# Kernel tuning notes

Measured on AMD Instinct MI355X. Metric: run time of the kernel, lower is better.

Reference implementation:

```python
import jax, jax.numpy as jnp
import numpy as np

B, S, D_IN, D_OUT = 8, 2048, 1024, 1024


def setup_inputs() -> dict:
    key = jax.random.key(0)
    kx, kq, kk, kv = jax.random.split(key, 4)
    x = jax.random.normal(kx, (B, S, D_IN), dtype=jnp.float32)
    # torch nn.Linear weight is (d_out, d_in); we store the transpose (d_in, d_out)
    # and apply as x @ W, same math. Scale ~ kaiming-uniform-ish magnitude.
    scale = 1.0 / np.sqrt(D_IN)
    Wq = jax.random.normal(kq, (D_IN, D_OUT), dtype=jnp.float32) * scale
    Wk = jax.random.normal(kk, (D_IN, D_OUT), dtype=jnp.float32) * scale
    Wv = jax.random.normal(kv, (D_IN, D_OUT), dtype=jnp.float32) * scale
    return {"x": x, "Wq": Wq, "Wk": Wk, "Wv": Wv}


def reference(x, Wq, Wk, Wv):
    # x: (b, s, d_in) -> (b, s, d_out). Single-head causal attention, dropout=0.
    b, s, _ = x.shape
    q = jnp.einsum('bsd,de->bse', x, Wq)
    k = jnp.einsum('bsd,de->bse', x, Wk)
    v = jnp.einsum('bsd,de->bse', x, Wv)
    d_k = k.shape[-1]
    scores = jnp.einsum('bqe,bke->bqk', q, k) / jnp.sqrt(jnp.float32(d_k))
    # causal mask: position t attends to 0..t (strict upper triangle -> -inf)
    causal = jnp.tril(jnp.ones((s, s), dtype=bool))
    scores = jnp.where(causal[None, :, :], scores, -jnp.inf)
    weights = jax.nn.softmax(scores, axis=-1)
    return jnp.einsum('bqk,bke->bqe', weights, v)
```

## Files before the change

### kernel.cpp

```cpp
#include <hip/hip_runtime.h>


#define Bv 8
#define Sv 2048
#define Dv 1024
#define BK 32

typedef _Float16 f16x8 __attribute__((ext_vector_type(8)));
typedef _Float16 f16x4 __attribute__((ext_vector_type(4)));
typedef float    f32x4 __attribute__((ext_vector_type(4)));

#define GLL(gp, lp)                                            \
  __builtin_amdgcn_global_load_lds(                            \
      (const __attribute__((address_space(1))) void*)(gp),     \
      (__attribute__((address_space(3))) void*)(lp), 16, 0, 0)

__device__ __forceinline__ void mma_step(const _Float16* As, const _Float16* Bs,
                                         int wm, int wn, int lane, f32x4 acc[4][4]) {
  int ll = lane & 15, quad = lane >> 4;
  f16x8 a[4], b[4];
#pragma unroll
  for (int mi = 0; mi < 4; ++mi)
    a[mi] = *(const f16x8*)(As + (wm * 64 + mi * 16 + ll) * BK + quad * 8);
#pragma unroll
  for (int ni = 0; ni < 4; ++ni)
    b[ni] = *(const f16x8*)(Bs + (wn * 64 + ni * 16 + ll) * BK + quad * 8);
#pragma unroll
  for (int mi = 0; mi < 4; ++mi)
#pragma unroll
    for (int ni = 0; ni < 4; ++ni)
      acc[mi][ni] = __builtin_amdgcn_mfma_f32_16x16x32_f16(a[mi], b[ni], acc[mi][ni], 0, 0, 0);
}

__device__ __forceinline__ void gemm_dbuf(const _Float16* __restrict__ A, int lda,
                                          const _Float16* __restrict__ B, int ldb,
                                          int ktiles, _Float16 (*S)[4096],
                                          f32x4 acc[4][4]) {
  const int tid  = threadIdx.x;
  const int lane = tid & 63, wave = tid >> 6;
  const int wm = wave >> 1, wn = wave & 1;
  const int srow = wave * 32 + (lane >> 2);
  const int scol = (lane & 3) * 8;
  const int loA0 = srow * lda + scol, loA1 = loA0 + 16 * lda;
  const int loB0 = srow * ldb + scol, loB1 = loB0 + 16 * ldb;
  _Float16* dA = &S[0][wave * 1024];
  _Float16* dB = &S[1][wave * 1024];
  const _Float16* gA = A;
  const _Float16* gB = B;

#define STAGE(bi)                              \
  do {                                         \
    GLL(gA + loA0, dA + (bi) * 8192);          \
    GLL(gA + loA1, dA + (bi) * 8192 + 512);    \
    GLL(gB + loB0, dB + (bi) * 8192);          \
    GLL(gB + loB1, dB + (bi) * 8192 + 512);    \
  } while (0)

  STAGE(0);
  for (int kt = 0; kt < ktiles; kt += 2) {
    __syncthreads();
    gA += BK; gB += BK;
    STAGE(1);
    mma_step(S[0], S[1], wm, wn, lane, acc);
    __syncthreads();
    gA += BK; gB += BK;
    if (kt + 2 < ktiles) STAGE(0);
    mma_step(S[2], S[3], wm, wn, lane, acc);
  }
#undef STAGE
}

#define ZERO_ACC(acc)                              \
  _Pragma("unroll") for (int i_ = 0; i_ < 4; ++i_) \
  _Pragma("unroll") for (int j_ = 0; j_ < 4; ++j_) \
      acc[i_][j_] = (f32x4){0.f, 0.f, 0.f, 0.f};

__global__ __launch_bounds__(256) void ca_cast(const float* __restrict__ x,
                                               _Float16* __restrict__ y) {
  int i = (blockIdx.x * 256 + threadIdx.x) * 8;
  f32x4 a = *(const f32x4*)(x + i);
  f32x4 b = *(const f32x4*)(x + i + 4);
  f16x8 h;
#pragma unroll
  for (int j = 0; j < 4; ++j) { h[j] = (_Float16)a[j]; h[4 + j] = (_Float16)b[j]; }
  *(f16x8*)(y + i) = h;
}

__global__ __launch_bounds__(256) void ca_transpose(const float* __restrict__ W0,
                                                    const float* __restrict__ W1,
                                                    const float* __restrict__ W2,
                                                    _Float16* __restrict__ T0,
                                                    _Float16* __restrict__ T1,
                                                    _Float16* __restrict__ T2) {
  const float* W = blockIdx.z == 0 ? W0 : blockIdx.z == 1 ? W1 : W2;
  _Float16* WT   = blockIdx.z == 0 ? T0 : blockIdx.z == 1 ? T1 : T2;
  __shared__ _Float16 t[32][33];
  int k0 = blockIdx.x * 32, n0 = blockIdx.y * 32;
  int r = threadIdx.x >> 5, c = threadIdx.x & 31;
#pragma unroll
  for (int i = 0; i < 4; ++i)
    t[r + i * 8][c] = (_Float16)W[(size_t)(k0 + r + i * 8) * Dv + n0 + c];
  __syncthreads();
#pragma unroll
  for (int i = 0; i < 4; ++i)
    WT[(size_t)(n0 + r + i * 8) * Dv + k0 + c] = t[c][r + i * 8];
}

__global__ __launch_bounds__(256) void ca_qkv(const _Float16* __restrict__ X,
                                              const _Float16* __restrict__ WTq,
                                              const _Float16* __restrict__ WTk,
                                              const _Float16* __restrict__ WTv,
                                              _Float16* __restrict__ Q,
                                              _Float16* __restrict__ K,
                                              _Float16* __restrict__ Vt) {
  __shared__ _Float16 S[4][4096];
  f32x4 acc[4][4];
  ZERO_ACC(acc);
  int nt = blockIdx.x;
  int m0 = blockIdx.y * 128;
  int which = nt >> 3;
  int n0 = (nt & 7) * 128;
  const _Float16* WT = which == 0 ? WTq : which == 1 ? WTk : WTv;
  gemm_dbuf(X + (size_t)m0 * Dv, Dv, WT + (size_t)n0 * Dv, Dv, Dv / BK, S, acc);
  int lane = threadIdx.x & 63, wave = threadIdx.x >> 6;
  int wm = wave >> 1, wn = wave & 1, ll = lane & 15, quad = lane >> 4;
  if (which < 2) {
    _Float16* Out = which == 0 ? Q : K;
#pragma unroll
    for (int mi = 0; mi < 4; ++mi)
#pragma unroll
      for (int ni = 0; ni < 4; ++ni) {
        int gc = n0 + wn * 64 + ni * 16 + ll;
#pragma unroll
        for (int r = 0; r < 4; ++r) {
          int gr = m0 + wm * 64 + mi * 16 + quad * 4 + r;
          Out[(size_t)gr * Dv + gc] = (_Float16)acc[mi][ni][r];
        }
      }
  } else {
#pragma unroll
    for (int mi = 0; mi < 4; ++mi)
#pragma unroll
      for (int ni = 0; ni < 4; ++ni) {
        int gc = n0 + wn * 64 + ni * 16 + ll;
        int gr = m0 + wm * 64 + mi * 16 + quad * 4;
        f16x4 v;
#pragma unroll
        for (int r = 0; r < 4; ++r) v[r] = (_Float16)acc[mi][ni][r];
        *(f16x4*)(Vt + (size_t)gc * (Bv * Sv) + gr) = v;
      }
  }
}

__global__ __launch_bounds__(256) void ca_score(const _Float16* __restrict__ Q,
                                                const _Float16* __restrict__ Km,
                                                _Float16* __restrict__ U) {
  int kt = blockIdx.x, qt = blockIdx.y, b = blockIdx.z;
  if (kt > qt) return;
  __shared__ _Float16 S[4][4096];
  f32x4 acc[4][4];
  ZERO_ACC(acc);
  const _Float16* Qb = Q + ((size_t)b * Sv + qt * 128) * Dv;
  const _Float16* Kb = Km + ((size_t)b * Sv + kt * 128) * Dv;
  gemm_dbuf(Qb, Dv, Kb, Dv, Dv / BK, S, acc);
  int lane = threadIdx.x & 63, wave = threadIdx.x >> 6;
  int wm = wave >> 1, wn = wave & 1, ll = lane & 15, quad = lane >> 4;
#pragma unroll
  for (int mi = 0; mi < 4; ++mi)
#pragma unroll
    for (int ni = 0; ni < 4; ++ni) {
      int kc = kt * 128 + wn * 64 + ni * 16 + ll;
#pragma unroll
      for (int r = 0; r < 4; ++r) {
        int qr = qt * 128 + wm * 64 + mi * 16 + quad * 4 + r;
        float s = acc[mi][ni][r] * 0.03125f;
        float u = (kc > qr) ? 0.f : __expf(fminf(fmaxf(s, -15.f), 10.f));
        U[((size_t)b * Sv + qr) * Sv + kc] = (_Float16)u;
      }
    }
}

__global__ __launch_bounds__(256) void ca_rowsum(const _Float16* __restrict__ U,
                                                 float* __restrict__ invl) {
  int rg = blockIdx.x;
  int b = rg >> 11, q = rg & (Sv - 1);
  int lim = ((q >> 7) + 1) << 7;
  const _Float16* row = U + ((size_t)b * Sv + q) * Sv;
  float s = 0.f;
  for (int k = threadIdx.x * 8; k < lim; k += 2048) {
    f16x8 v = *(const f16x8*)(row + k);
#pragma unroll
    for (int j = 0; j < 8; ++j) s += (float)v[j];
  }
#pragma unroll
  for (int o = 32; o >= 1; o >>= 1) s += __shfl_down(s, o);
  __shared__ float wsum[4];
  if ((threadIdx.x & 63) == 0) wsum[threadIdx.x >> 6] = s;
  __syncthreads();
  if (threadIdx.x == 0) invl[rg] = 1.f / (wsum[0] + wsum[1] + wsum[2] + wsum[3]);
}

__global__ __launch_bounds__(256) void ca_pv(const _Float16* __restrict__ U,
                                             const _Float16* __restrict__ Vt,
                                             const float* __restrict__ invl,
                                             float* __restrict__ Out) {
  int nt = blockIdx.x, qt = blockIdx.y, b = blockIdx.z;
  __shared__ _Float16 S[4][4096];
  f32x4 acc[4][4];
  ZERO_ACC(acc);
  const _Float16* Ab = U + ((size_t)b * Sv + qt * 128) * Sv;
  const _Float16* Bb = Vt + (size_t)(nt * 128) * (Bv * Sv) + (size_t)b * Sv;
  gemm_dbuf(Ab, Sv, Bb, Bv * Sv, (qt + 1) * 4, S, acc);
  int lane = threadIdx.x & 63, wave = threadIdx.x >> 6;
  int wm = wave >> 1, wn = wave & 1, ll = lane & 15, quad = lane >> 4;
#pragma unroll
  for (int mi = 0; mi < 4; ++mi)
#pragma unroll
    for (int ni = 0; ni < 4; ++ni) {
      int oc = nt * 128 + wn * 64 + ni * 16 + ll;
#pragma unroll
      for (int r = 0; r < 4; ++r) {
        int qr = qt * 128 + wm * 64 + mi * 16 + quad * 4 + r;
        Out[((size_t)b * Sv + qr) * Dv + oc] = acc[mi][ni][r] * invl[b * Sv + qr];
      }
    }
}

extern "C" void kernel_launch(void* const* d_in, const int* in_sizes, int n_in,
                              void* d_out, int out_size, void* d_ws, size_t ws_size,
                              hipStream_t stream) {
  const float* x  = (const float*)d_in[0];
  const float* Wq = (const float*)d_in[1];
  const float* Wk = (const float*)d_in[2];
  const float* Wv = (const float*)d_in[3];
  float* out = (float*)d_out;

  char* ws = (char*)d_ws;
  size_t off = 0;
  const size_t M = (size_t)Bv * Sv;
  _Float16* xh  = (_Float16*)(ws + off); off += M * Dv * 2;
  _Float16* WTq = (_Float16*)(ws + off); off += (size_t)Dv * Dv * 2;
  _Float16* WTk = (_Float16*)(ws + off); off += (size_t)Dv * Dv * 2;
  _Float16* WTv = (_Float16*)(ws + off); off += (size_t)Dv * Dv * 2;
  _Float16* Q   = (_Float16*)(ws + off); off += M * Dv * 2;
  _Float16* Km  = (_Float16*)(ws + off); off += M * Dv * 2;
  _Float16* Vt  = (_Float16*)(ws + off); off += M * Dv * 2;
  _Float16* U   = (_Float16*)(ws + off); off += (size_t)Bv * Sv * Sv * 2;
  float*    invl = (float*)(ws + off);   off += M * 4;

  ca_cast<<<(M * Dv) / (8 * 256), 256, 0, stream>>>(x, xh);
  ca_transpose<<<dim3(32, 32, 3), 256, 0, stream>>>(Wq, Wk, Wv, WTq, WTk, WTv);

  ca_qkv<<<dim3(24, M / 128), 256, 0, stream>>>(xh, WTq, WTk, WTv, Q, Km, Vt);

  ca_score<<<dim3(Sv / 128, Sv / 128, Bv), 256, 0, stream>>>(Q, Km, U);
  ca_rowsum<<<M, 256, 0, stream>>>(U, invl);
  ca_pv<<<dim3(Dv / 128, Sv / 128, Bv), 256, 0, stream>>>(U, Vt, invl, out);
}
```

Baseline: 429.6 us.

## Rewrite QKV projection GEMM with 256x256 tiles, 4-stage LDS pipeline and swizzle

Replaces the 128x128, 256-thread QKV projection kernel with a 512-thread kernel computing 256x256 output tiles. It streams operands through a 4-deep ring of LDS buffers via direct global-to-LDS loads, uses XOR-swizzled LDS addressing to avoid bank conflicts, raises wave priority around the MFMA block, and remaps block indices so neighbouring blocks share operand tiles in cache. The aim is more arithmetic per loaded byte and better hiding of memory latency in the largest GEMM. In exchange it uses far more LDS and registers (64 KB LDS, 128 accumulator floats per thread), which may limit occupancy.

```diff
diff --git a/kernel.cpp b/kernel.cpp
--- a/kernel.cpp
+++ b/kernel.cpp
@@ -5,6 +5,7 @@
 #define Sv 2048
 #define Dv 1024
 #define BK 32
+#define NKT (Dv / BK)
 
 typedef _Float16 f16x8 __attribute__((ext_vector_type(8)));
 typedef _Float16 f16x4 __attribute__((ext_vector_type(4)));
@@ -106,44 +107,107 @@
     WT[(size_t)(n0 + r + i * 8) * Dv + k0 + c] = t[c][r + i * 8];
 }
 
-__global__ __launch_bounds__(256) void ca_qkv(const _Float16* __restrict__ X,
-                                              const _Float16* __restrict__ WTq,
-                                              const _Float16* __restrict__ WTk,
-                                              const _Float16* __restrict__ WTv,
-                                              _Float16* __restrict__ Q,
-                                              _Float16* __restrict__ K,
-                                              _Float16* __restrict__ Vt) {
-  __shared__ _Float16 S[4][4096];
-  f32x4 acc[4][4];
-  ZERO_ACC(acc);
-  int nt = blockIdx.x;
-  int m0 = blockIdx.y * 128;
-  int which = nt >> 3;
-  int n0 = (nt & 7) * 128;
+__global__ __launch_bounds__(512, 2) void ca_qkv2(const _Float16* __restrict__ X,
+                                                  const _Float16* __restrict__ WTq,
+                                                  const _Float16* __restrict__ WTk,
+                                                  const _Float16* __restrict__ WTv,
+                                                  _Float16* __restrict__ Q,
+                                                  _Float16* __restrict__ K,
+                                                  _Float16* __restrict__ Vt) {
+  __shared__ _Float16 As[4][256 * BK];
+  __shared__ _Float16 Bs[4][256 * BK];
+
+  int id  = blockIdx.x;
+  int swz = (id & 7) * 96 + (id >> 3);
+  int my  = swz / 12, nt = swz - my * 12;
+  int m0  = my * 256;
+  int which = nt >> 2;
+  int n0  = (nt & 3) * 256;
   const _Float16* WT = which == 0 ? WTq : which == 1 ? WTk : WTv;
-  gemm_dbuf(X + (size_t)m0 * Dv, Dv, WT + (size_t)n0 * Dv, Dv, Dv / BK, S, acc);
-  int lane = threadIdx.x & 63, wave = threadIdx.x >> 6;
-  int wm = wave >> 1, wn = wave & 1, ll = lane & 15, quad = lane >> 4;
+  const _Float16* gA = X + (size_t)m0 * Dv;
+  const _Float16* gB = WT + (size_t)n0 * Dv;
+
+  const int tid  = threadIdx.x;
+  const int lane = tid & 63, wave = tid >> 6;
+  const int wm = wave >> 2, wn = wave & 3;
+  const int ll = lane & 15, quad = lane >> 4;
+  const int cw   = (lane >> 1) & 3;
+  const int cofs = (quad ^ cw) << 3;
+  const int aoff = (wm * 128 + ll) * BK + cofs;
+  const int boff = (wn * 64 + ll) * BK + cofs;
+  const int srow = wave * 32 + (lane >> 2);
+  const int scol = (((lane & 3) ^ ((lane >> 3) & 3)) << 3);
+  const int loA0 = srow * Dv + scol, loA1 = loA0 + 16 * Dv;
+
+#define QSTAGE(ktp, p)                              \
+  do {                                              \
+    const _Float16* ga_ = gA + (ktp) * BK;          \
+    const _Float16* gb_ = gB + (ktp) * BK;          \
+    GLL(ga_ + loA0, &As[p][wave * 1024]);           \
+    GLL(ga_ + loA1, &As[p][wave * 1024 + 512]);     \
+    GLL(gb_ + loA0, &Bs[p][wave * 1024]);           \
+    GLL(gb_ + loA1, &Bs[p][wave * 1024 + 512]);     \
+  } while (0)
+
+  f32x4 acc[8][4];
+#pragma unroll
+  for (int i = 0; i < 8; ++i)
+#pragma unroll
+    for (int j = 0; j < 4; ++j) acc[i][j] = (f32x4){0.f, 0.f, 0.f, 0.f};
+
+  QSTAGE(0, 0); QSTAGE(1, 1); QSTAGE(2, 2);
+
+#define QSTEP(ktc, p)                                                         \
+  do {                                                                        \
+    asm volatile("s_waitcnt vmcnt(8)" ::: "memory");                          \
+    __builtin_amdgcn_s_barrier();                                             \
+    __builtin_amdgcn_sched_barrier(0);                                        \
+    if ((ktc) + 3 < NKT) QSTAGE((ktc) + 3, ((p) + 3) & 3);                    \
+    const _Float16* Ap_ = As[p];                                              \
+    const _Float16* Bp_ = Bs[p];                                              \
+    f16x8 a_[8], b_[4];                                                       \
+    _Pragma("unroll") for (int mi = 0; mi < 8; ++mi)                          \
+        a_[mi] = *(const f16x8*)(Ap_ + aoff + mi * (16 * BK));                \
+    _Pragma("unroll") for (int ni = 0; ni < 4; ++ni)                          \
+        b_[ni] = *(const f16x8*)(Bp_ + boff + ni * (16 * BK));                \
+    __builtin_amdgcn_s_setprio(1);                                            \
+    _Pragma("unroll") for (int mi = 0; mi < 8; ++mi)                          \
+      _Pragma("unroll") for (int ni = 0; ni < 4; ++ni)                        \
+          acc[mi][ni] = __builtin_amdgcn_mfma_f32_16x16x32_f16(               \
+              a_[mi], b_[ni], acc[mi][ni], 0, 0, 0);                          \
+    __builtin_amdgcn_s_setprio(0);                                            \
+  } while (0)
+
+#pragma unroll 1
+  for (int kt = 0; kt < NKT; kt += 4) {
+    QSTEP(kt + 0, 0);
+    QSTEP(kt + 1, 1);
+    QSTEP(kt + 2, 2);
+    QSTEP(kt + 3, 3);
+  }
+#undef QSTEP
+#undef QSTAGE
+
   if (which < 2) {
     _Float16* Out = which == 0 ? Q : K;
 #pragma unroll
-    for (int mi = 0; mi < 4; ++mi)
+    for (int mi = 0; mi < 8; ++mi)
 #pragma unroll
       for (int ni = 0; ni < 4; ++ni) {
         int gc = n0 + wn * 64 + ni * 16 + ll;
 #pragma unroll
         for (int r = 0; r < 4; ++r) {
-          int gr = m0 + wm * 64 + mi * 16 + quad * 4 + r;
+          int gr = m0 + wm * 128 + mi * 16 + quad * 4 + r;
           Out[(size_t)gr * Dv + gc] = (_Float16)acc[mi][ni][r];
         }
       }
   } else {
 #pragma unroll
-    for (int mi = 0; mi < 4; ++mi)
+    for (int mi = 0; mi < 8; ++mi)
 #pragma unroll
       for (int ni = 0; ni < 4; ++ni) {
         int gc = n0 + wn * 64 + ni * 16 + ll;
-        int gr = m0 + wm * 64 + mi * 16 + quad * 4;
+        int gr = m0 + wm * 128 + mi * 16 + quad * 4;
         f16x4 v;
 #pragma unroll
         for (int r = 0; r < 4; ++r) v[r] = (_Float16)acc[mi][ni][r];
@@ -251,7 +315,7 @@
   ca_cast<<<(M * Dv) / (8 * 256), 256, 0, stream>>>(x, xh);
   ca_transpose<<<dim3(32, 32, 3), 256, 0, stream>>>(Wq, Wk, Wv, WTq, WTk, WTv);
 
-  ca_qkv<<<dim3(24, M / 128), 256, 0, stream>>>(xh, WTq, WTk, WTv, Q, Km, Vt);
+  ca_qkv2<<<dim3(768), 512, 0, stream>>>(xh, WTq, WTk, WTv, Q, Km, Vt);
 
   ca_score<<<dim3(Sv / 128, Sv / 128, Bv), 256, 0, stream>>>(Q, Km, U);
   ca_rowsum<<<M, 256, 0, stream>>>(U, invl);
```

Result: faster. 413.8 us (-3.7%).

## Rewrite QKV projection GEMM with 256x256 tiles and phased LDS pipeline

Applied to the files above, without the earlier changes.

Replaces the 128x128-tile QKV projection kernel with a 512-thread, 256x256-tile GEMM. It uses a swizzled block index for L2 locality and XOR-swizzled LDS layouts to avoid bank conflicts. Global-to-LDS loads are interleaved in four sub-phases per K-step, with explicit barriers, waitcnts and setprio around MFMA bursts to overlap memory and compute. The larger tiles raise arithmetic intensity but use more registers and LDS and make the synchronisation harder to get right. A dead first MMA macro definition is left in and then undefined.

```diff
diff --git a/kernel.cpp b/kernel.cpp
--- a/kernel.cpp
+++ b/kernel.cpp
@@ -5,6 +5,7 @@
 #define Sv 2048
 #define Dv 1024
 #define BK 32
+#define NT 16
 
 typedef _Float16 f16x8 __attribute__((ext_vector_type(8)));
 typedef _Float16 f16x4 __attribute__((ext_vector_type(4)));
@@ -106,44 +107,150 @@
     WT[(size_t)(n0 + r + i * 8) * Dv + k0 + c] = t[c][r + i * 8];
 }
 
-__global__ __launch_bounds__(256) void ca_qkv(const _Float16* __restrict__ X,
-                                              const _Float16* __restrict__ WTq,
-                                              const _Float16* __restrict__ WTk,
-                                              const _Float16* __restrict__ WTv,
-                                              _Float16* __restrict__ Q,
-                                              _Float16* __restrict__ K,
-                                              _Float16* __restrict__ Vt) {
-  __shared__ _Float16 S[4][4096];
-  f32x4 acc[4][4];
-  ZERO_ACC(acc);
-  int nt = blockIdx.x;
-  int m0 = blockIdx.y * 128;
-  int which = nt >> 3;
-  int n0 = (nt & 7) * 128;
+__global__ __launch_bounds__(512, 2) void ca_qkv3(const _Float16* __restrict__ X,
+                                                  const _Float16* __restrict__ WTq,
+                                                  const _Float16* __restrict__ WTk,
+                                                  const _Float16* __restrict__ WTv,
+                                                  _Float16* __restrict__ Q,
+                                                  _Float16* __restrict__ K,
+                                                  _Float16* __restrict__ Vt) {
+  __shared__ _Float16 L[8][8192];
+
+  int id  = blockIdx.x;
+  int swz = (id & 7) * 96 + (id >> 3);
+  int my  = swz / 12, nt = swz - my * 12;
+  int m0  = my * 256;
+  int which = nt >> 2;
+  int n0  = (nt & 3) * 256;
   const _Float16* WT = which == 0 ? WTq : which == 1 ? WTk : WTv;
-  gemm_dbuf(X + (size_t)m0 * Dv, Dv, WT + (size_t)n0 * Dv, Dv, Dv / BK, S, acc);
-  int lane = threadIdx.x & 63, wave = threadIdx.x >> 6;
-  int wm = wave >> 1, wn = wave & 1, ll = lane & 15, quad = lane >> 4;
+  const _Float16* gA = X + (size_t)m0 * Dv;
+  const _Float16* gB = WT + (size_t)n0 * Dv;
+
+  const int tid  = threadIdx.x;
+  const int lane = tid & 63, wave = tid >> 6;
+  const int wm = wave >> 2, wn = wave & 3;
+  const int ll = lane & 15, quad = lane >> 4;
+
+  const int laneRow = wave * 8 + (lane >> 3);
+  const int laneCol = (((lane & 7) ^ ((lane >> 3) & 7)) << 3);
+  const int gOff0 = laneRow * Dv + laneCol;
+  const int gOff1 = (64 + laneRow) * Dv + laneCol;
+  _Float16* Ldst = &L[0][0] + wave * 512;
+
+  const int sw0 = ((quad ^ (ll & 7)) << 3);
+  _Float16* Lb = &L[0][0];
+  const _Float16* pA0 = Lb + wm * 8192 + ll * 64 + sw0;
+  const _Float16* pA1 = Lb + wm * 8192 + ll * 64 + (sw0 ^ 32);
+  const _Float16* pB0 = Lb + 16384 + (wn >> 1) * 8192 + (wn & 1) * 4096 + ll * 64 + sw0;
+  const _Float16* pB1 = Lb + 16384 + (wn >> 1) * 8192 + (wn & 1) * 4096 + ll * 64 + (sw0 ^ 32);
+
+#define STG(slot, mat, ht, kpf)                                   \
+  do {                                                            \
+    const _Float16* g_ = (mat) + (size_t)((ht) * 128 * Dv + (kpf) * 64); \
+    GLL(g_ + gOff0, Ldst + (slot) * 8192);                        \
+    GLL(g_ + gOff1, Ldst + (slot) * 8192 + 4096);                 \
+  } while (0)
+
+#define RD_A(P, d, mh)                                            \
+  _Pragma("unroll") for (int i_ = 0; i_ < 4; ++i_)                \
+      a[i_] = *(const f16x8*)((P) + (d) * 32768 + ((mh) * 4 + i_) * 1024);
+#define RD_B(P, d)                                                \
+  _Pragma("unroll") for (int i_ = 0; i_ < 4; ++i_)                \
+      b[i_] = *(const f16x8*)((P) + (d) * 32768 + i_ * 1024);
+#define MMA(mh)                                                   \
+  __builtin_amdgcn_s_setprio(1);                                  \
+  _Pragma("unroll") for (int i_ = 0; i_ < 4; ++i_)                \
+  _Pragma("unroll") for (int j_ = 0; j_ < 4; ++j_)                \
+      acc[(mh) * 4 + i_][j_] = __builtin_amdgcn_mfma_f32_16x16x32_f16( \
+          a[i_], b[j_], acc[(mh) * 4 + i_], 0, 0, 0)[0] == 0.f    \
+          ? __builtin_amdgcn_mfma_f32_16x16x32_f16(a[i_], b[j_], acc[(mh) * 4 + i_][j_], 0, 0, 0) \
+          : __builtin_amdgcn_mfma_f32_16x16x32_f16(a[i_], b[j_], acc[(mh) * 4 + i_][j_], 0, 0, 0); \
+  __builtin_amdgcn_s_setprio(0);
+#undef MMA
+#define MMA(mh)                                                   \
+  __builtin_amdgcn_s_setprio(1);                                  \
+  _Pragma("unroll") for (int i_ = 0; i_ < 4; ++i_)                \
+  _Pragma("unroll") for (int j_ = 0; j_ < 4; ++j_)                \
+      acc[(mh) * 4 + i_][j_] = __builtin_amdgcn_mfma_f32_16x16x32_f16( \
+          a[i_], b[j_], acc[(mh) * 4 + i_][j_], 0, 0, 0);         \
+  __builtin_amdgcn_s_setprio(0);
+#define BAR() __builtin_amdgcn_s_barrier()
+#define WAITV_(n) asm volatile("s_waitcnt vmcnt(" #n ")" ::: "memory")
+#define WAITV(n) WAITV_(n)
+#define PH_OPEN()                                                 \
+  BAR();                                                          \
+  asm volatile("s_waitcnt lgkmcnt(0)" ::: "memory");              \
+  __builtin_amdgcn_sched_barrier(0)
+
+#define TILEG(kk, d, G)                                           \
+  do {                                                            \
+    f16x8 a[4], b[4];                                             \
+    RD_A(pA0, d, 0); RD_B(pB0, d);                                \
+    if ((kk) + 1 < NT) STG(4 * (1 - (d)) + 0, gA, 0, (kk) + 1);   \
+    PH_OPEN(); MMA(0); BAR();                                     \
+    RD_A(pA0, d, 1);                                              \
+    if ((kk) + 1 < NT) STG(4 * (1 - (d)) + 1, gA, 1, (kk) + 1);   \
+    PH_OPEN(); MMA(1); BAR();                                     \
+    RD_A(pA1, d, 0); RD_B(pB1, d);                                \
+    if ((kk) + 1 < NT) STG(4 * (1 - (d)) + 3, gB, 1, (kk) + 1);   \
+    PH_OPEN(); MMA(0); BAR();                                     \
+    __builtin_amdgcn_sched_barrier(0);                            \
+    RD_A(pA1, d, 1);                                              \
+    if ((kk) + 2 < NT) STG(4 * (d) + 2, gB, 0, (kk) + 2);         \
+    PH_OPEN(); MMA(1);                                            \
+    WAITV(G); BAR();                                              \
+    __builtin_amdgcn_sched_barrier(0);                            \
+  } while (0)
+
+  f32x4 acc[8][4];
+#pragma unroll
+  for (int i = 0; i < 8; ++i)
+#pragma unroll
+    for (int j = 0; j < 4; ++j) acc[i][j] = (f32x4){0.f, 0.f, 0.f, 0.f};
+
+  STG(2, gB, 0, 0);
+  STG(0, gA, 0, 0);
+  STG(1, gA, 1, 0);
+  STG(3, gB, 1, 0);
+  STG(6, gB, 0, 1);
+  WAITV(2); BAR();
+  __builtin_amdgcn_sched_barrier(0);
+
+#pragma unroll 1
+  for (int kk = 0; kk < NT - 2; kk += 2) {
+    TILEG(kk, 0, 2);
+    TILEG(kk + 1, 1, 2);
+  }
+  TILEG(14, 0, 0);
+  TILEG(15, 1, 2);
+
+#undef TILEG
+#undef PH_OPEN
+#undef MMA
+#undef RD_A
+#undef RD_B
+#undef STG
+
   if (which < 2) {
     _Float16* Out = which == 0 ? Q : K;
 #pragma unroll
-    for (int mi = 0; mi < 4; ++mi)
+    for (int mi = 0; mi < 8; ++mi)
 #pragma unroll
       for (int ni = 0; ni < 4; ++ni) {
         int gc = n0 + wn * 64 + ni * 16 + ll;
 #pragma unroll
         for (int r = 0; r < 4; ++r) {
-          int gr = m0 + wm * 64 + mi * 16 + quad * 4 + r;
+          int gr = m0 + wm * 128 + mi * 16 + quad * 4 + r;
           Out[(size_t)gr * Dv + gc] = (_Float16)acc[mi][ni][r];
         }
       }
   } else {
 #pragma unroll
-    for (int mi = 0; mi < 4; ++mi)
+    for (int mi = 0; mi < 8; ++mi)
 #pragma unroll
       for (int ni = 0; ni < 4; ++ni) {
         int gc = n0 + wn * 64 + ni * 16 + ll;
-        int gr = m0 + wm * 64 + mi * 16 + quad * 4;
+        int gr = m0 + wm * 128 + mi * 16 + quad * 4;
         f16x4 v;
 #pragma unroll
         for (int r = 0; r < 4; ++r) v[r] = (_Float16)acc[mi][ni][r];
@@ -251,7 +358,7 @@
   ca_cast<<<(M * Dv) / (8 * 256), 256, 0, stream>>>(x, xh);
   ca_transpose<<<dim3(32, 32, 3), 256, 0, stream>>>(Wq, Wk, Wv, WTq, WTk, WTv);
 
-  ca_qkv<<<dim3(24, M / 128), 256, 0, stream>>>(xh, WTq, WTk, WTv, Q, Km, Vt);
+  ca_qkv3<<<dim3(768), 512, 0, stream>>>(xh, WTq, WTk, WTv, Q, Km, Vt);
 
   ca_score<<<dim3(Sv / 128, Sv / 128, Bv), 256, 0, stream>>>(Q, Km, U);
   ca_rowsum<<<M, 256, 0, stream>>>(U, invl);
```

Measured after the change: 405.2 us. 1.06x faster.
